# Optimization experiments

Measured on AMD Instinct MI355X. Metric: run time of the kernel, lower is better.

Reference implementation:

```python
import jax, jax.numpy as jnp
import numpy as np
from math import sqrt

B, N, D = 8, 4096, 512

def rotary(x, phases):
    # x: [B,N,D], phases: [B,N,D/2]
    c, s = jnp.cos(phases), jnp.sin(phases)
    a, b = jnp.split(x, 2, axis=-1)
    return jnp.concatenate([a * c - b * s, a * s + b * c], axis=-1)

def setup_inputs() -> dict:
    key = jax.random.key(0)
    ks = jax.random.split(key, 8)
    phi = jax.random.normal(ks[0], (B, N, D), dtype=jnp.float32)
    coords = jax.random.normal(ks[1], (B, N, 3), dtype=jnp.float32)
    weights = jax.random.uniform(ks[2], (B, N), dtype=jnp.float32)
    std = 1.0 / sqrt(D)
    Wq = jax.random.normal(ks[3], (D, D), dtype=jnp.float32) * std
    Wk = jax.random.normal(ks[4], (D, D), dtype=jnp.float32) * std
    Wv = jax.random.normal(ks[5], (D, D), dtype=jnp.float32) * std
    bq = jnp.zeros((D,), jnp.float32)
    bk = jnp.zeros((D,), jnp.float32)
    bv = jnp.zeros((D,), jnp.float32)
    # mode_lift weight, std = 1/kernel_scale with kernel_scale=1.0
    Wrot = jax.random.normal(ks[6], (D // 2, 3), dtype=jnp.float32)
    return {"phi": phi, "coords": coords, "weights": weights,
            "Wq": Wq, "bq": bq, "Wk": Wk, "bk": bk, "Wv": Wv, "bv": bv,
            "Wrot": Wrot}

def reference(phi, coords, weights, Wq, bq, Wk, bk, Wv, bv, Wrot):
    d = phi.shape[-1]
    q = phi @ Wq.T + bq
    k = phi @ Wk.T + bk
    v = phi @ Wv.T + bv
    # _normalize: scale query by 1/sqrt(d); attach quadrature weights to value
    q = q * (1.0 / sqrt(d))
    v = weights[..., None] * v
    # rotary positional encoding on q and k
    phases = jnp.einsum('bnc,dc->bnd', coords, Wrot)  # [B,N,D/2]
    q = rotary(q, phases)
    k = rotary(k, phases)
    # linear attention: q @ (k^T @ v), O(N*d^2)
    kv = jnp.einsum('bnd,bne->bde', k, v)   # [B,D,D]
    return jnp.einsum('bnd,bde->bne', q, kv)  # [B,N,D]
```

## Files before the change

### kernel.cpp

```cpp
#include <hip/hip_runtime.h>


typedef _Float16 f16x8 __attribute__((ext_vector_type(8)));
typedef _Float16 f16x4 __attribute__((ext_vector_type(4)));
typedef float f32x4 __attribute__((ext_vector_type(4)));

__device__ __forceinline__ void gl_lds16(const void* g, void* l) {
    __builtin_amdgcn_global_load_lds(
        (const __attribute__((address_space(1))) void*)g,
        (__attribute__((address_space(3))) void*)l, 16, 0, 0);
}

__global__ __launch_bounds__(256) void convert_phi(const float* __restrict__ phi,
                                                   _Float16* __restrict__ phi_h) {
    int i = (blockIdx.x * 256 + threadIdx.x) * 4;
    float4 v = *(const float4*)(phi + i);
    f16x4 o = {(_Float16)v.x, (_Float16)v.y, (_Float16)v.z, (_Float16)v.w};
    *(f16x4*)(phi_h + i) = o;
}

__global__ __launch_bounds__(256) void pack_w(
    const float* __restrict__ Wq, const float* __restrict__ Wk,
    const float* __restrict__ Wv, const float* __restrict__ bq,
    const float* __restrict__ bk, const float* __restrict__ bv,
    _Float16* __restrict__ wcat, float* __restrict__ bcat) {
    int j = blockIdx.x;
    int reg = j >> 9, jr = j & 511;
    const float* W; const float* bias;
    if (reg == 0)      { W = Wq; bias = bq; }
    else if (reg == 1) { W = Wk; bias = bk; }
    else               { W = Wv; bias = bv; }
    int d = (reg < 2) ? ((jr & 1) ? (jr >> 1) + 256 : (jr >> 1)) : jr;
    for (int i = threadIdx.x; i < 512; i += 256)
        wcat[j * 512 + i] = (_Float16)W[d * 512 + i];
    if (threadIdx.x == 0) bcat[j] = bias[d];
}

__global__ __launch_bounds__(256) void qkv_kernel(
    const _Float16* __restrict__ phi_h, const _Float16* __restrict__ wcat,
    const float* __restrict__ bcat, const float* __restrict__ coords,
    const float* __restrict__ weights, const float* __restrict__ Wrot,
    _Float16* __restrict__ qr, _Float16* __restrict__ krT,
    _Float16* __restrict__ vwT) {
    __shared__ __align__(16) char smem[34816];
    _Float16* As = (_Float16*)smem;
    _Float16* Bs = (_Float16*)(smem + 8192);
    _Float16* Ts = (_Float16*)smem;

    const int tid = threadIdx.x;
    const int lane = tid & 63, wave = tid >> 6;
    const int quad = lane >> 4, l16 = lane & 15;
    const int wm = (wave >> 1) * 64, wn = (wave & 1) * 64;
    const int m0 = blockIdx.y * 128;
    const int c0 = blockIdx.x * 128;

    const int ca = wave * 2;
    const int srow = lane >> 2, sseg = (lane & 3) * 8;

    f32x4 acc[4][4] = {};

    for (int k0 = 0; k0 < 512; k0 += 32) {
        #pragma unroll
        for (int c = 0; c < 2; c++) {
            int chunk = ca + c;
            int row = chunk * 16 + srow;
            gl_lds16(&phi_h[(m0 + row) * 512 + k0 + sseg], &As[chunk * 512]);
            gl_lds16(&wcat[(c0 + row) * 512 + k0 + sseg], &Bs[chunk * 512]);
        }
        __syncthreads();
        f16x8 af[4], bf[4];
        #pragma unroll
        for (int mi = 0; mi < 4; mi++)
            af[mi] = *(f16x8*)&As[(wm + mi * 16 + l16) * 32 + quad * 8];
        #pragma unroll
        for (int ni = 0; ni < 4; ni++)
            bf[ni] = *(f16x8*)&Bs[(wn + ni * 16 + l16) * 32 + quad * 8];
        #pragma unroll
        for (int mi = 0; mi < 4; mi++)
            #pragma unroll
            for (int ni = 0; ni < 4; ni++)
                acc[mi][ni] = __builtin_amdgcn_mfma_f32_16x16x32_f16(
                    af[mi], bf[ni], acc[mi][ni], 0, 0, 0);
        __syncthreads();
    }

    const int region = c0 >> 9;
    const float qscale = 0.04419417382415922f;

    float bias[4], w0[4], w1[4], w2[4];
    #pragma unroll
    for (int ni = 0; ni < 4; ni++) {
        int gc = c0 + wn + ni * 16 + l16;
        bias[ni] = bcat[gc];
        if (region < 2) {
            int jp = (gc & 511) >> 1;
            w0[ni] = Wrot[jp * 3];
            w1[ni] = Wrot[jp * 3 + 1];
            w2[ni] = Wrot[jp * 3 + 2];
        }
    }

    if (region == 0) {
        #pragma unroll
        for (int mi = 0; mi < 4; mi++)
            #pragma unroll
            for (int r = 0; r < 4; r++) {
                int row = wm + mi * 16 + quad * 4 + r;
                int gm = m0 + row;
                float x = coords[gm * 3], y = coords[gm * 3 + 1], z = coords[gm * 3 + 2];
                #pragma unroll
                for (int ni = 0; ni < 4; ni++) {
                    float val = (acc[mi][ni][r] + bias[ni]) * qscale;
                    float part = __shfl_xor(val, 1);
                    float ph = x * w0[ni] + y * w1[ni] + z * w2[ni];
                    float sv, cv; __sincosf(ph, &sv, &cv);
                    float res = (l16 & 1) ? (part * sv + val * cv)
                                          : (val * cv - part * sv);
                    Ts[row * 136 + wn + ni * 16 + l16] = (_Float16)res;
                }
            }
        __syncthreads();
        for (int i = tid; i < 2048; i += 256) {
            int row = i >> 4, cv = (i & 15) * 8;
            *(f16x8*)&qr[(m0 + row) * 512 + c0 + cv] = *(f16x8*)&Ts[row * 136 + cv];
        }
    } else {
        #pragma unroll
        for (int mi = 0; mi < 4; mi++)
            #pragma unroll
            for (int r = 0; r < 4; r++) {
                int row = wm + mi * 16 + quad * 4 + r;
                int gm = m0 + row;
                if (region == 1) {
                    float x = coords[gm * 3], y = coords[gm * 3 + 1], z = coords[gm * 3 + 2];
                    #pragma unroll
                    for (int ni = 0; ni < 4; ni++) {
                        float val = acc[mi][ni][r] + bias[ni];
                        float part = __shfl_xor(val, 1);
                        float ph = x * w0[ni] + y * w1[ni] + z * w2[ni];
                        float sv, cv; __sincosf(ph, &sv, &cv);
                        float res = (l16 & 1) ? (part * sv + val * cv)
                                              : (val * cv - part * sv);
                        Ts[(wn + ni * 16 + l16) * 136 + row] = (_Float16)res;
                    }
                } else {
                    float wgt = weights[gm];
                    #pragma unroll
                    for (int ni = 0; ni < 4; ni++) {
                        float val = (acc[mi][ni][r] + bias[ni]) * wgt;
                        Ts[(wn + ni * 16 + l16) * 136 + row] = (_Float16)val;
                    }
                }
            }
        __syncthreads();
        _Float16* dst = (region == 1) ? krT : vwT;
        const int b = m0 >> 12, n0 = m0 & 4095, cb = c0 & 511;
        for (int i = tid; i < 2048; i += 256) {
            int col = i >> 4, rv = (i & 15) * 8;
            *(f16x8*)&dst[((size_t)b * 512 + cb + col) * 4096 + n0 + rv] =
                *(f16x8*)&Ts[col * 136 + rv];
        }
    }
}

__global__ __launch_bounds__(256) void kv_kernel(
    const _Float16* __restrict__ vwT, const _Float16* __restrict__ krT,
    float* __restrict__ kvp) {
    __shared__ __align__(16) _Float16 As[128 * 32];
    __shared__ __align__(16) _Float16 Bs[128 * 32];
    const int tid = threadIdx.x, lane = tid & 63, wave = tid >> 6;
    const int quad = lane >> 4, l16 = lane & 15;
    const int wm = (wave >> 1) * 64, wn = (wave & 1) * 64;
    const int d0 = blockIdx.x * 128, e0 = blockIdx.y * 128;
    const int b = blockIdx.z >> 2, split = blockIdx.z & 3;
    const size_t base = (size_t)b * 512 * 4096;
    const int kbeg = split * 1024, kend = kbeg + 1024;
    const int ca = wave * 2;
    const int srow = lane >> 2, sseg = (lane & 3) * 8;
    f32x4 acc[4][4] = {};
    for (int k0 = kbeg; k0 < kend; k0 += 32) {
        #pragma unroll
        for (int c = 0; c < 2; c++) {
            int chunk = ca + c;
            int row = chunk * 16 + srow;
            gl_lds16(&vwT[base + (size_t)(e0 + row) * 4096 + k0 + sseg], &As[chunk * 512]);
            gl_lds16(&krT[base + (size_t)(d0 + row) * 4096 + k0 + sseg], &Bs[chunk * 512]);
        }
        __syncthreads();
        f16x8 af[4], bf[4];
        #pragma unroll
        for (int mi = 0; mi < 4; mi++)
            af[mi] = *(f16x8*)&As[(wm + mi * 16 + l16) * 32 + quad * 8];
        #pragma unroll
        for (int ni = 0; ni < 4; ni++)
            bf[ni] = *(f16x8*)&Bs[(wn + ni * 16 + l16) * 32 + quad * 8];
        #pragma unroll
        for (int mi = 0; mi < 4; mi++)
            #pragma unroll
            for (int ni = 0; ni < 4; ni++)
                acc[mi][ni] = __builtin_amdgcn_mfma_f32_16x16x32_f16(
                    af[mi], bf[ni], acc[mi][ni], 0, 0, 0);
        __syncthreads();
    }
    float* dst = kvp + ((size_t)split * 8 + b) * 262144;
    #pragma unroll
    for (int mi = 0; mi < 4; mi++)
        #pragma unroll
        for (int ni = 0; ni < 4; ni++)
            #pragma unroll
            for (int r = 0; r < 4; r++) {
                int e = e0 + wm + mi * 16 + quad * 4 + r;
                int d = d0 + wn + ni * 16 + l16;
                dst[e * 512 + d] = acc[mi][ni][r];
            }
}

__global__ __launch_bounds__(256) void reduce_kv(const float* __restrict__ kvp,
                                                 _Float16* __restrict__ kvT) {
    int i = (blockIdx.x * 256 + threadIdx.x) * 4;
    f32x4 s = *(const f32x4*)(kvp + i);
    s += *(const f32x4*)(kvp + 2097152 + i);
    s += *(const f32x4*)(kvp + 4194304 + i);
    s += *(const f32x4*)(kvp + 6291456 + i);
    f16x4 o = {(_Float16)s.x, (_Float16)s.y, (_Float16)s.z, (_Float16)s.w};
    *(f16x4*)(kvT + i) = o;
}

__global__ __launch_bounds__(256) void out_kernel(
    const _Float16* __restrict__ qr, const _Float16* __restrict__ kvT,
    float* __restrict__ out) {
    __shared__ __align__(16) _Float16 As[128 * 32];
    __shared__ __align__(16) _Float16 Bs[128 * 32];
    const int tid = threadIdx.x, lane = tid & 63, wave = tid >> 6;
    const int quad = lane >> 4, l16 = lane & 15;
    const int wm = (wave >> 1) * 64, wn = (wave & 1) * 64;
    const int m0 = blockIdx.y * 128, e0 = blockIdx.x * 128;
    const int b = m0 >> 12;
    const int ca = wave * 2;
    const int srow = lane >> 2, sseg = (lane & 3) * 8;
    f32x4 acc[4][4] = {};
    for (int k0 = 0; k0 < 512; k0 += 32) {
        #pragma unroll
        for (int c = 0; c < 2; c++) {
            int chunk = ca + c;
            int row = chunk * 16 + srow;
            gl_lds16(&qr[(m0 + row) * 512 + k0 + sseg], &As[chunk * 512]);
            gl_lds16(&kvT[(size_t)b * 262144 + (e0 + row) * 512 + k0 + sseg],
                     &Bs[chunk * 512]);
        }
        __syncthreads();
        f16x8 af[4], bf[4];
        #pragma unroll
        for (int mi = 0; mi < 4; mi++)
            af[mi] = *(f16x8*)&As[(wm + mi * 16 + l16) * 32 + quad * 8];
        #pragma unroll
        for (int ni = 0; ni < 4; ni++)
            bf[ni] = *(f16x8*)&Bs[(wn + ni * 16 + l16) * 32 + quad * 8];
        #pragma unroll
        for (int mi = 0; mi < 4; mi++)
            #pragma unroll
            for (int ni = 0; ni < 4; ni++)
                acc[mi][ni] = __builtin_amdgcn_mfma_f32_16x16x32_f16(
                    af[mi], bf[ni], acc[mi][ni], 0, 0, 0);
        __syncthreads();
    }
    #pragma unroll
    for (int mi = 0; mi < 4; mi++)
        #pragma unroll
        for (int ni = 0; ni < 4; ni++)
            #pragma unroll
            for (int r = 0; r < 4; r++) {
                int gm = m0 + wm + mi * 16 + quad * 4 + r;
                int e = e0 + wn + ni * 16 + l16;
                out[(size_t)gm * 512 + e] = acc[mi][ni][r];
            }
}

extern "C" void kernel_launch(void* const* d_in, const int* in_sizes, int n_in,
                              void* d_out, int out_size, void* d_ws, size_t ws_size,
                              hipStream_t stream) {
    const float* phi     = (const float*)d_in[0];
    const float* coords  = (const float*)d_in[1];
    const float* weights = (const float*)d_in[2];
    const float* Wq      = (const float*)d_in[3];
    const float* bq      = (const float*)d_in[4];
    const float* Wk      = (const float*)d_in[5];
    const float* bk      = (const float*)d_in[6];
    const float* Wv      = (const float*)d_in[7];
    const float* bv      = (const float*)d_in[8];
    const float* Wrot    = (const float*)d_in[9];
    float* out = (float*)d_out;

    char* ws = (char*)d_ws;
    _Float16* phi_h = (_Float16*)(ws);
    float*    kvp   = (float*)   (ws);
    _Float16* wcat  = (_Float16*)(ws + 33554432);
    float*    bcat  = (float*)   (ws + 35127296);
    _Float16* qr    = (_Float16*)(ws + 35133440);
    _Float16* krT   = (_Float16*)(ws + 68687872);
    _Float16* vwT   = (_Float16*)(ws + 102242304);
    _Float16* kvT   = (_Float16*)(ws + 135796736);

    convert_phi<<<16384, 256, 0, stream>>>(phi, phi_h);
    pack_w<<<1536, 256, 0, stream>>>(Wq, Wk, Wv, bq, bk, bv, wcat, bcat);
    qkv_kernel<<<dim3(12, 256), 256, 0, stream>>>(phi_h, wcat, bcat, coords,
                                                  weights, Wrot, qr, krT, vwT);
    kv_kernel<<<dim3(4, 4, 32), 256, 0, stream>>>(vwT, krT, kvp);
    reduce_kv<<<2048, 256, 0, stream>>>(kvp, kvT);
    out_kernel<<<dim3(4, 256), 256, 0, stream>>>(qr, kvT, out);
}
```

Baseline: 326.3 us.

## Double-buffer LDS in GEMM kernels, split kv into 8 fp16 partials

Adds double-buffered LDS staging to the qkv, kv and out GEMM kernels so that global-to-LDS loads of the next K slice overlap with MFMA work on the current one, while keeping one barrier per slice. The kv reduction is split into 8 K-chunks instead of 4 to launch more blocks, and the partial results are stored in fp16 instead of fp32, which halves partial-buffer traffic for the reduce kernel. The trade-off is more LDS per block, which may lower occupancy, and some precision loss from rounding the partial sums to fp16 before they are added.

After: 319.7 us. 2.0% less time.

```diff
diff --git a/kernel.cpp b/kernel.cpp
--- a/kernel.cpp
+++ b/kernel.cpp
@@ -9,6 +9,34 @@
     __builtin_amdgcn_global_load_lds(
         (const __attribute__((address_space(1))) void*)g,
         (__attribute__((address_space(3))) void*)l, 16, 0, 0);
+}
+
+__device__ __forceinline__ void stage2(const _Float16* gA, size_t sA,
+                                       const _Float16* gB, size_t sB,
+                                       _Float16* As, _Float16* Bs,
+                                       int ca, int srow, int sseg) {
+    gl_lds16(&gA[(size_t)(ca * 16 + srow) * sA + sseg], &As[ca * 512]);
+    gl_lds16(&gA[(size_t)(ca * 16 + 16 + srow) * sA + sseg], &As[(ca + 1) * 512]);
+    gl_lds16(&gB[(size_t)(ca * 16 + srow) * sB + sseg], &Bs[ca * 512]);
+    gl_lds16(&gB[(size_t)(ca * 16 + 16 + srow) * sB + sseg], &Bs[(ca + 1) * 512]);
+}
+
+__device__ __forceinline__ void mfma_step(const _Float16* As, const _Float16* Bs,
+                                          int wm, int wn, int l16, int quad,
+                                          f32x4 acc[4][4]) {
+    f16x8 af[4], bf[4];
+    #pragma unroll
+    for (int mi = 0; mi < 4; mi++)
+        af[mi] = *(const f16x8*)&As[(wm + mi * 16 + l16) * 32 + quad * 8];
+    #pragma unroll
+    for (int ni = 0; ni < 4; ni++)
+        bf[ni] = *(const f16x8*)&Bs[(wn + ni * 16 + l16) * 32 + quad * 8];
+    #pragma unroll
+    for (int mi = 0; mi < 4; mi++)
+        #pragma unroll
+        for (int ni = 0; ni < 4; ni++)
+            acc[mi][ni] = __builtin_amdgcn_mfma_f32_16x16x32_f16(
+                af[mi], bf[ni], acc[mi][ni], 0, 0, 0);
 }
 
 __global__ __launch_bounds__(256) void convert_phi(const float* __restrict__ phi,
@@ -43,9 +71,11 @@
     _Float16* __restrict__ qr, _Float16* __restrict__ krT,
     _Float16* __restrict__ vwT) {
     __shared__ __align__(16) char smem[34816];
-    _Float16* As = (_Float16*)smem;
-    _Float16* Bs = (_Float16*)(smem + 8192);
-    _Float16* Ts = (_Float16*)smem;
+    _Float16* As0 = (_Float16*)smem;
+    _Float16* Bs0 = (_Float16*)(smem + 8192);
+    _Float16* As1 = (_Float16*)(smem + 16384);
+    _Float16* Bs1 = (_Float16*)(smem + 24576);
+    _Float16* Ts  = (_Float16*)smem;
 
     const int tid = threadIdx.x;
     const int lane = tid & 63, wave = tid >> 6;
@@ -53,34 +83,23 @@
     const int wm = (wave >> 1) * 64, wn = (wave & 1) * 64;
     const int m0 = blockIdx.y * 128;
     const int c0 = blockIdx.x * 128;
-
     const int ca = wave * 2;
     const int srow = lane >> 2, sseg = (lane & 3) * 8;
 
+    const _Float16* gA = phi_h + (size_t)m0 * 512;
+    const _Float16* gB = wcat + (size_t)c0 * 512;
+
     f32x4 acc[4][4] = {};
 
-    for (int k0 = 0; k0 < 512; k0 += 32) {
-        #pragma unroll
-        for (int c = 0; c < 2; c++) {
-            int chunk = ca + c;
-            int row = chunk * 16 + srow;
-            gl_lds16(&phi_h[(m0 + row) * 512 + k0 + sseg], &As[chunk * 512]);
-            gl_lds16(&wcat[(c0 + row) * 512 + k0 + sseg], &Bs[chunk * 512]);
-        }
-        __syncthreads();
-        f16x8 af[4], bf[4];
-        #pragma unroll
-        for (int mi = 0; mi < 4; mi++)
-            af[mi] = *(f16x8*)&As[(wm + mi * 16 + l16) * 32 + quad * 8];
-        #pragma unroll
-        for (int ni = 0; ni < 4; ni++)
-            bf[ni] = *(f16x8*)&Bs[(wn + ni * 16 + l16) * 32 + quad * 8];
-        #pragma unroll
-        for (int mi = 0; mi < 4; mi++)
-            #pragma unroll
-            for (int ni = 0; ni < 4; ni++)
-                acc[mi][ni] = __builtin_amdgcn_mfma_f32_16x16x32_f16(
-                    af[mi], bf[ni], acc[mi][ni], 0, 0, 0);
+    stage2(gA, 512, gB, 512, As0, Bs0, ca, srow, sseg);
+    __syncthreads();
+    for (int k0 = 0; k0 < 512; k0 += 64) {
+        stage2(gA + k0 + 32, 512, gB + k0 + 32, 512, As1, Bs1, ca, srow, sseg);
+        mfma_step(As0, Bs0, wm, wn, l16, quad, acc);
+        __syncthreads();
+        if (k0 + 64 < 512)
+            stage2(gA + k0 + 64, 512, gB + k0 + 64, 512, As0, Bs0, ca, srow, sseg);
+        mfma_step(As1, Bs1, wm, wn, l16, quad, acc);
         __syncthreads();
     }
 
@@ -165,44 +184,38 @@
 
 __global__ __launch_bounds__(256) void kv_kernel(
     const _Float16* __restrict__ vwT, const _Float16* __restrict__ krT,
-    float* __restrict__ kvp) {
-    __shared__ __align__(16) _Float16 As[128 * 32];
-    __shared__ __align__(16) _Float16 Bs[128 * 32];
+    _Float16* __restrict__ kvp) {
+    __shared__ __align__(16) char smem[32768];
+    _Float16* As0 = (_Float16*)smem;
+    _Float16* Bs0 = (_Float16*)(smem + 8192);
+    _Float16* As1 = (_Float16*)(smem + 16384);
+    _Float16* Bs1 = (_Float16*)(smem + 24576);
     const int tid = threadIdx.x, lane = tid & 63, wave = tid >> 6;
     const int quad = lane >> 4, l16 = lane & 15;
     const int wm = (wave >> 1) * 64, wn = (wave & 1) * 64;
     const int d0 = blockIdx.x * 128, e0 = blockIdx.y * 128;
-    const int b = blockIdx.z >> 2, split = blockIdx.z & 3;
-    const size_t base = (size_t)b * 512 * 4096;
-    const int kbeg = split * 1024, kend = kbeg + 1024;
+    const int b = blockIdx.z >> 3, split = blockIdx.z & 7;
     const int ca = wave * 2;
     const int srow = lane >> 2, sseg = (lane & 3) * 8;
+    const size_t base = (size_t)b * 512 * 4096;
+    const int kbeg = split * 512;
+    const _Float16* gA = vwT + base + (size_t)e0 * 4096 + kbeg;
+    const _Float16* gB = krT + base + (size_t)d0 * 4096 + kbeg;
     f32x4 acc[4][4] = {};
-    for (int k0 = kbeg; k0 < kend; k0 += 32) {
-        #pragma unroll
-        for (int c = 0; c < 2; c++) {
-            int chunk = ca + c;
-            int row = chunk * 16 + srow;
-            gl_lds16(&vwT[base + (size_t)(e0 + row) * 4096 + k0 + sseg], &As[chunk * 512]);
-            gl_lds16(&krT[base + (size_t)(d0 + row) * 4096 + k0 + sseg], &Bs[chunk * 512]);
-        }
-        __syncthreads();
-        f16x8 af[4], bf[4];
-        #pragma unroll
-        for (int mi = 0; mi < 4; mi++)
-            af[mi] = *(f16x8*)&As[(wm + mi * 16 + l16) * 32 + quad * 8];
-        #pragma unroll
-        for (int ni = 0; ni < 4; ni++)
-            bf[ni] = *(f16x8*)&Bs[(wn + ni * 16 + l16) * 32 + quad * 8];
-        #pragma unroll
-        for (int mi = 0; mi < 4; mi++)
-            #pragma unroll
-            for (int ni = 0; ni < 4; ni++)
-                acc[mi][ni] = __builtin_amdgcn_mfma_f32_16x16x32_f16(
-                    af[mi], bf[ni], acc[mi][ni], 0, 0, 0);
-        __syncthreads();
-    }
-    float* dst = kvp + ((size_t)split * 8 + b) * 262144;
+
+    stage2(gA, 4096, gB, 4096, As0, Bs0, ca, srow, sseg);
+    __syncthreads();
+    for (int k0 = 0; k0 < 512; k0 += 64) {
+        stage2(gA + k0 + 32, 4096, gB + k0 + 32, 4096, As1, Bs1, ca, srow, sseg);
+        mfma_step(As0, Bs0, wm, wn, l16, quad, acc);
+        __syncthreads();
+        if (k0 + 64 < 512)
+            stage2(gA + k0 + 64, 4096, gB + k0 + 64, 4096, As0, Bs0, ca, srow, sseg);
+        mfma_step(As1, Bs1, wm, wn, l16, quad, acc);
+        __syncthreads();
+    }
+
+    _Float16* dst = kvp + ((size_t)split * 8 + b) * 262144;
     #pragma unroll
     for (int mi = 0; mi < 4; mi++)
         #pragma unroll
@@ -211,26 +224,34 @@
             for (int r = 0; r < 4; r++) {
                 int e = e0 + wm + mi * 16 + quad * 4 + r;
                 int d = d0 + wn + ni * 16 + l16;
-                dst[e * 512 + d] = acc[mi][ni][r];
+                dst[e * 512 + d] = (_Float16)acc[mi][ni][r];
             }
 }
 
-__global__ __launch_bounds__(256) void reduce_kv(const float* __restrict__ kvp,
+__global__ __launch_bounds__(256) void reduce_kv(const _Float16* __restrict__ kvp,
                                                  _Float16* __restrict__ kvT) {
-    int i = (blockIdx.x * 256 + threadIdx.x) * 4;
-    f32x4 s = *(const f32x4*)(kvp + i);
-    s += *(const f32x4*)(kvp + 2097152 + i);
-    s += *(const f32x4*)(kvp + 4194304 + i);
-    s += *(const f32x4*)(kvp + 6291456 + i);
-    f16x4 o = {(_Float16)s.x, (_Float16)s.y, (_Float16)s.z, (_Float16)s.w};
-    *(f16x4*)(kvT + i) = o;
+    int i = (blockIdx.x * 256 + threadIdx.x) * 8;
+    float s[8] = {};
+    #pragma unroll
+    for (int sp = 0; sp < 8; sp++) {
+        f16x8 v = *(const f16x8*)(kvp + (size_t)sp * 2097152 + i);
+        #pragma unroll
+        for (int j = 0; j < 8; j++) s[j] += (float)v[j];
+    }
+    f16x8 o;
+    #pragma unroll
+    for (int j = 0; j < 8; j++) o[j] = (_Float16)s[j];
+    *(f16x8*)(kvT + i) = o;
 }
 
 __global__ __launch_bounds__(256) void out_kernel(
     const _Float16* __restrict__ qr, const _Float16* __restrict__ kvT,
     float* __restrict__ out) {
-    __shared__ __align__(16) _Float16 As[128 * 32];
-    __shared__ __align__(16) _Float16 Bs[128 * 32];
+    __shared__ __align__(16) char smem[32768];
+    _Float16* As0 = (_Float16*)smem;
+    _Float16* Bs0 = (_Float16*)(smem + 8192);
+    _Float16* As1 = (_Float16*)(smem + 16384);
+    _Float16* Bs1 = (_Float16*)(smem + 24576);
     const int tid = threadIdx.x, lane = tid & 63, wave = tid >> 6;
     const int quad = lane >> 4, l16 = lane & 15;
     const int wm = (wave >> 1) * 64, wn = (wave & 1) * 64;
@@ -238,32 +259,22 @@
     const int b = m0 >> 12;
     const int ca = wave * 2;
     const int srow = lane >> 2, sseg = (lane & 3) * 8;
+    const _Float16* gA = qr + (size_t)m0 * 512;
+    const _Float16* gB = kvT + (size_t)b * 262144 + (size_t)e0 * 512;
     f32x4 acc[4][4] = {};
-    for (int k0 = 0; k0 < 512; k0 += 32) {
-        #pragma unroll
-        for (int c = 0; c < 2; c++) {
-            int chunk = ca + c;
-            int row = chunk * 16 + srow;
-            gl_lds16(&qr[(m0 + row) * 512 + k0 + sseg], &As[chunk * 512]);
-            gl_lds16(&kvT[(size_t)b * 262144 + (e0 + row) * 512 + k0 + sseg],
-                     &Bs[chunk * 512]);
-        }
-        __syncthreads();
-        f16x8 af[4], bf[4];
-        #pragma unroll
-        for (int mi = 0; mi < 4; mi++)
-            af[mi] = *(f16x8*)&As[(wm + mi * 16 + l16) * 32 + quad * 8];
-        #pragma unroll
-        for (int ni = 0; ni < 4; ni++)
-            bf[ni] = *(f16x8*)&Bs[(wn + ni * 16 + l16) * 32 + quad * 8];
-        #pragma unroll
-        for (int mi = 0; mi < 4; mi++)
-            #pragma unroll
-            for (int ni = 0; ni < 4; ni++)
-                acc[mi][ni] = __builtin_amdgcn_mfma_f32_16x16x32_f16(
-                    af[mi], bf[ni], acc[mi][ni], 0, 0, 0);
-        __syncthreads();
-    }
+
+    stage2(gA, 512, gB, 512, As0, Bs0, ca, srow, sseg);
+    __syncthreads();
+    for (int k0 = 0; k0 < 512; k0 += 64) {
+        stage2(gA + k0 + 32, 512, gB + k0 + 32, 512, As1, Bs1, ca, srow, sseg);
+        mfma_step(As0, Bs0, wm, wn, l16, quad, acc);
+        __syncthreads();
+        if (k0 + 64 < 512)
+            stage2(gA + k0 + 64, 512, gB + k0 + 64, 512, As0, Bs0, ca, srow, sseg);
+        mfma_step(As1, Bs1, wm, wn, l16, quad, acc);
+        __syncthreads();
+    }
+
     #pragma unroll
     for (int mi = 0; mi < 4; mi++)
         #pragma unroll
@@ -293,7 +304,7 @@
 
     char* ws = (char*)d_ws;
     _Float16* phi_h = (_Float16*)(ws);
-    float*    kvp   = (float*)   (ws);
+    _Float16* kvp   = (_Float16*)(ws);
     _Float16* wcat  = (_Float16*)(ws + 33554432);
     float*    bcat  = (float*)   (ws + 35127296);
     _Float16* qr    = (_Float16*)(ws + 35133440);
@@ -305,7 +316,7 @@
     pack_w<<<1536, 256, 0, stream>>>(Wq, Wk, Wv, bq, bk, bv, wcat, bcat);
     qkv_kernel<<<dim3(12, 256), 256, 0, stream>>>(phi_h, wcat, bcat, coords,
                                                   weights, Wrot, qr, krT, vwT);
-    kv_kernel<<<dim3(4, 4, 32), 256, 0, stream>>>(vwT, krT, kvp);
-    reduce_kv<<<2048, 256, 0, stream>>>(kvp, kvT);
+    kv_kernel<<<dim3(4, 4, 64), 256, 0, stream>>>(vwT, krT, kvp);
+    reduce_kv<<<1024, 256, 0, stream>>>(kvp, kvT);
     out_kernel<<<dim3(4, 256), 256, 0, stream>>>(qr, kvT, out);
 }
```
